# Optimization experiments

Measured on AMD Instinct MI355X. Metric: run time of the kernel, lower is better.

Reference implementation:

```python
import jax, jax.numpy as jnp
import numpy as np

B, T, D_IN, H1, H2, K = 16, 1024, 384, 1024, 1024, 9


def _l2normalize(w, axis):
    # matches F.normalize(w, dim=axis): w / max(||w||_2, 1e-12)
    n = jnp.sqrt(jnp.sum(w * w, axis=axis, keepdims=True))
    return w / jnp.maximum(n, 1e-12)


def _mish(x):
    return x * jnp.tanh(jax.nn.softplus(x))


def setup_inputs() -> dict:
    key = jax.random.key(0)
    ks = jax.random.split(key, 11)
    f32 = jnp.float32
    return {
        "input": jax.random.normal(ks[0], (B, T, D_IN), f32),
        "d_w": jax.random.normal(ks[1], (B, H1, 1, K), f32),
        "d_g": jax.random.normal(ks[2], (B, H1), f32),
        "d_b": jax.random.normal(ks[3], (B, H1), f32),
        "p_w": jax.random.normal(ks[4], (B, H1, H2, 1), f32),
        "p_g": jax.random.normal(ks[5], (B, H1), f32),
        "p_b": jax.random.normal(ks[6], (B, H2), f32),
        "w1_w": jax.random.normal(ks[7], (H1, D_IN), f32) * 0.05,
        "w1_b": jax.random.normal(ks[8], (H1,), f32) * 0.05,
        "w2_w": jax.random.normal(ks[9], (D_IN, H2), f32) * 0.05,
        "w2_b": jax.random.normal(ks[10], (D_IN,), f32) * 0.05,
    }


def reference(input, d_w, d_g, d_b, p_w, p_g, p_b, w1_w, w1_b, w2_w, w2_b):
    residual = input
    # w_1: 1x1 conv == per-position linear, then Mish (dropout = identity in eval)
    h = _mish(jnp.einsum('btc,hc->bth', input, w1_w) + w1_b)   # [B,T,H1]
    x = jnp.transpose(h, (0, 2, 1))                            # [B,H1,T]
    k = d_w.shape[-1]
    pad = (k - 1) // 2
    t = x.shape[-1]
    xp = jnp.pad(x, ((0, 0), (0, 0), (pad, pad)))              # [B,H1,T+2p]
    idx = jnp.arange(t)[:, None] + jnp.arange(k)[None, :]      # [T,K]
    xu = xp[:, :, idx]                                         # [B,H1,T,K] (unfold)
    # weight-normalized dynamic depthwise conv weights
    dwn = _l2normalize(d_w, axis=1) * d_g[:, :, None, None]    # [B,H1,1,K]
    # torch.einsum('bctk,bcwk->bct') with d_w expanded along w(=T): w is summed,
    # and every w-slice is identical, so the dot product picks up a factor of T.
    y = jnp.einsum('bctk,bck->bct', xu, dwn[:, :, 0, :]) * t   # [B,H1,T]
    y = y + d_b[:, :, None]
    # weight-normalized dynamic pointwise mix
    pwn = _l2normalize(p_w, axis=1) * p_g[:, :, None, None]    # [B,H1,H2,1]
    z = jnp.einsum('bct,bco->bot', y, pwn[..., 0])             # [B,H2,T]
    z = z + p_b[:, :, None]
    # w_2: 1x1 conv back to d_in, residual add
    out2 = jnp.einsum('bot,do->btd', z, w2_w) + w2_b           # [B,T,D_IN]
    return out2 + residual
```

## Files before the change

### kernel.cpp

```cpp
#include <hip/hip_runtime.h>

#define BCNT 16
#define TT 1024
#define DIN 384
#define H1 1024
#define H2 1024
#define KW 9

typedef __attribute__((ext_vector_type(8))) short bhalf8;
typedef __attribute__((ext_vector_type(4))) float f32x4;

typedef const __attribute__((address_space(1))) void* gas_ptr;
typedef __attribute__((address_space(3))) void* lds_ptr;

__device__ __forceinline__ float bf2f(unsigned short u) {
    return __uint_as_float(((unsigned int)u) << 16);
}
__device__ __forceinline__ unsigned short f2bf(float f) {
    unsigned int u = __float_as_uint(f);
    unsigned int r = (u + 0x7FFFu + ((u >> 16) & 1u)) >> 16;
    return (unsigned short)r;
}
__device__ __forceinline__ float mish_f(float x) {
    if (x > 20.f) return x;
    float u = __expf(x);
    float n = u * u + 2.f * u;
    return x * n / (n + 2.f);
}


__global__ __launch_bounds__(256) void k_cvt3z(
    const float* __restrict__ s0, unsigned short* __restrict__ d0, int n0,
    const float* __restrict__ s1, unsigned short* __restrict__ d1, int n1,
    const float* __restrict__ s2, unsigned short* __restrict__ d2, int n2,
    float* __restrict__ zb, int n3) {
    int i = blockIdx.x * 256 + threadIdx.x;
    const float* s; unsigned short* d; int j = i;
    if (i < n0) { s = s0; d = d0; }
    else if ((j = i - n0) < n1) { s = s1; d = d1; }
    else if ((j = i - n0 - n1) < n2) { s = s2; d = d2; }
    else if ((j = i - n0 - n1 - n2) < n3) {
        ((float4*)zb)[j] = make_float4(0.f, 0.f, 0.f, 0.f);
        return;
    } else return;
    float4 v = ((const float4*)s)[j];
    ushort4 o;
    o.x = f2bf(v.x); o.y = f2bf(v.y); o.z = f2bf(v.z); o.w = f2bf(v.w);
    ((ushort4*)d)[j] = o;
}

__global__ void k_norm_dwn(const float* __restrict__ d_w, const float* __restrict__ d_g,
                           float* __restrict__ dwn_s) {
    int idx = blockIdx.x;
    int b = idx / KW, k = idx % KW;
    float s = 0.f;
    for (int c = threadIdx.x; c < H1; c += 256) {
        float v = d_w[((size_t)b * H1 + c) * KW + k];
        s += v * v;
    }
    __shared__ float red[256];
    __shared__ float nsh;
    red[threadIdx.x] = s; __syncthreads();
    for (int st = 128; st > 0; st >>= 1) {
        if (threadIdx.x < st) red[threadIdx.x] += red[threadIdx.x + st];
        __syncthreads();
    }
    if (threadIdx.x == 0) nsh = fmaxf(sqrtf(red[0]), 1e-12f);
    __syncthreads();
    float n = nsh;
    for (int c = threadIdx.x; c < H1; c += 256) {
        size_t o = ((size_t)b * H1 + c) * KW + k;
        dwn_s[o] = d_w[o] / n * d_g[b * H1 + c] * (float)TT;
    }
}

__global__ __launch_bounds__(256) void k_tpw2(const float* __restrict__ p_w,
                                              const float* __restrict__ p_g,
                                              unsigned short* __restrict__ pwTu,
                                              float* __restrict__ sumsq) {
    __shared__ float tile[32][33];
    __shared__ float red[8][32];
    int tx = threadIdx.x & 31, ty = threadIdx.x >> 5;
    int c0 = blockIdx.x * 32, o0 = blockIdx.y * 32, b = blockIdx.z;
    float s = 0.f;
#pragma unroll
    for (int j = 0; j < 4; j++) {
        float v = p_w[((size_t)b * H1 + c0 + ty + j * 8) * H2 + o0 + tx];
        tile[ty + j * 8][tx] = v;
        s += v * v;
    }
    red[ty][tx] = s;
    __syncthreads();
    if (ty == 0) {
        float t = 0.f;
#pragma unroll
        for (int r = 0; r < 8; r++) t += red[r][tx];
        atomicAdd(&sumsq[(size_t)b * H2 + o0 + tx], t);
    }
#pragma unroll
    for (int j = 0; j < 4; j++) {
        int o = o0 + ty + j * 8, c = c0 + tx;
        float v = tile[tx][ty + j * 8] * p_g[(size_t)b * H1 + c];
        pwTu[((size_t)b * H2 + o) * H1 + c] = f2bf(v);
    }
}

__global__ __launch_bounds__(256) void k_conv(const unsigned short* __restrict__ h,
                                              const float* __restrict__ dwn_s,
                                              const float* __restrict__ d_b,
                                              unsigned short* __restrict__ y) {
    int tid = threadIdx.x;
    int c2 = blockIdx.y * 256 + tid;
    int c = c2 * 2;
    int t0 = blockIdx.x * 64;
    int b = blockIdx.z;
    const ushort2* hb = (const ushort2*)(h + (size_t)b * TT * H1);
    ushort2* yb = (ushort2*)(y + (size_t)b * TT * H1);
    float k0[KW], k1[KW];
#pragma unroll
    for (int i = 0; i < KW; i++) {
        k0[i] = dwn_s[((size_t)b * H1 + c) * KW + i];
        k1[i] = dwn_s[((size_t)b * H1 + c + 1) * KW + i];
    }
    float db0 = d_b[b * H1 + c], db1 = d_b[b * H1 + c + 1];
    float w0[KW], w1[KW];
#pragma unroll
    for (int i = 0; i < 8; i++) {
        int t = t0 - 4 + i;
        if (t >= 0 && t < TT) {
            ushort2 v = hb[(size_t)t * (H1 / 2) + c2];
            w0[i] = bf2f(v.x); w1[i] = bf2f(v.y);
        } else { w0[i] = 0.f; w1[i] = 0.f; }
    }
    for (int j = 0; j < 64; j++) {
        int t = t0 + j;
        int tl = t + 4;
        if (tl < TT) {
            ushort2 v = hb[(size_t)tl * (H1 / 2) + c2];
            w0[8] = bf2f(v.x); w1[8] = bf2f(v.y);
        } else { w0[8] = 0.f; w1[8] = 0.f; }
        float a0 = db0, a1 = db1;
#pragma unroll
        for (int i = 0; i < KW; i++) { a0 += k0[i] * w0[i]; a1 += k1[i] * w1[i]; }
        ushort2 o; o.x = f2bf(a0); o.y = f2bf(a1);
        yb[(size_t)t * (H1 / 2) + c2] = o;
#pragma unroll
        for (int i = 0; i < 8; i++) { w0[i] = w0[i + 1]; w1[i] = w1[i + 1]; }
    }
}

template <int MODE, int SWIZ, int TN>
__global__ __launch_bounds__(256, 4) void gemm_nt(
    const unsigned short* __restrict__ A, const unsigned short* __restrict__ Bm,
    void* __restrict__ Cp, int Kdim, int lda, int ldb, int ldc,
    long sA, long sB, long sC,
    const float* __restrict__ bias, int biasStride,
    const float* __restrict__ sumsq,
    const unsigned short* __restrict__ residbf) {
    constexpr int WN = TN / 32;
    __shared__ __attribute__((aligned(16))) unsigned short Al[128 * 64];
    __shared__ __attribute__((aligned(16))) unsigned short Bl[TN * 64];

    const int tid = threadIdx.x;
    const int lane = tid & 63, wv = tid >> 6;

    int bx, by, bz;
    if constexpr (SWIZ) {
        int l = blockIdx.x;
        int xcd = l & 7, s = l >> 3;
        bz = xcd * 2 + (s >> 6);
        int u = s & 63;
        bx = u & 7; by = u >> 3;
    } else {
        bx = blockIdx.x; by = blockIdx.y; bz = blockIdx.z;
    }
    const int bm = bx * 128, bn = by * TN;

    const unsigned short* Ab = A + (size_t)sA * bz;
    const unsigned short* Bb = Bm + (size_t)sB * bz;

    const int rS = lane >> 3;
    const int cS = ((lane & 7) ^ (rS & 7)) * 8;

    const int wm = (wv >> 1) * 64, wn = (wv & 1) * (TN / 2);
    const int l16 = lane & 15, quad = lane >> 4;
    const int fx = l16 & 7;

    f32x4 acc[4][WN];
#pragma unroll
    for (int i = 0; i < 4; i++)
#pragma unroll
        for (int j = 0; j < WN; j++)
#pragma unroll
            for (int r = 0; r < 4; r++) acc[i][j][r] = 0.f;

    const int ktiles = Kdim / 64;
    for (int kt = 0; kt < ktiles; ++kt) {
        const int kofs = kt * 64 + cS;
#pragma unroll
        for (int i = 0; i < 4; i++) {
            const int ch = i * 4 + wv;
            const unsigned short* ga = Ab + (size_t)(bm + ch * 8 + rS) * lda + kofs;
            __builtin_amdgcn_global_load_lds((gas_ptr)ga, (lds_ptr)&Al[ch * 512], 16, 0, 0);
        }
#pragma unroll
        for (int i = 0; i < TN / 32; i++) {
            const int ch = i * 4 + wv;
            const unsigned short* gb = Bb + (size_t)(bn + ch * 8 + rS) * ldb + kofs;
            __builtin_amdgcn_global_load_lds((gas_ptr)gb, (lds_ptr)&Bl[ch * 512], 16, 0, 0);
        }
        __syncthreads();

#pragma unroll
        for (int kk = 0; kk < 2; kk++) {
            const int cg = ((kk * 4 + quad) ^ fx) * 8;
            bhalf8 af[4], bf[WN];
#pragma unroll
            for (int mi = 0; mi < 4; mi++)
                af[mi] = *(const bhalf8*)&Al[(wm + mi * 16 + l16) * 64 + cg];
#pragma unroll
            for (int ni = 0; ni < WN; ni++)
                bf[ni] = *(const bhalf8*)&Bl[(wn + ni * 16 + l16) * 64 + cg];
#pragma unroll
            for (int mi = 0; mi < 4; mi++)
#pragma unroll
                for (int ni = 0; ni < WN; ni++)
                    acc[mi][ni] = __builtin_amdgcn_mfma_f32_16x16x32_bf16(af[mi], bf[ni],
                                                                         acc[mi][ni], 0, 0, 0);
        }
        __syncthreads();
    }

#pragma unroll
    for (int mi = 0; mi < 4; mi++)
#pragma unroll
        for (int ni = 0; ni < WN; ni++)
#pragma unroll
            for (int r = 0; r < 4; r++) {
                int gm = bm + wm + mi * 16 + quad * 4 + r;
                int gn = bn + wn + ni * 16 + l16;
                float v = acc[mi][ni][r];
                size_t cidx = (size_t)sC * bz + (size_t)gm * ldc + gn;
                if constexpr (MODE == 0) {
                    v = mish_f(v + bias[gn]);
                    ((unsigned short*)Cp)[cidx] = f2bf(v);
                } else if constexpr (MODE == 1) {
                    size_t si = (size_t)bz * biasStride + gn;
                    float rr = rsqrtf(fmaxf(sumsq[si], 1e-24f));
                    v = v * rr + bias[si];
                    ((unsigned short*)Cp)[cidx] = f2bf(v);
                } else {
                    v += bias[gn] + bf2f(residbf[cidx]);
                    ((float*)Cp)[cidx] = v;
                }
            }
}


extern "C" void kernel_launch(void* const* d_in, const int* in_sizes, int n_in,
                              void* d_out, int out_size, void* d_ws, size_t ws_size,
                              hipStream_t stream) {
    const float* input = (const float*)d_in[0];
    const float* d_w   = (const float*)d_in[1];
    const float* d_g   = (const float*)d_in[2];
    const float* d_b   = (const float*)d_in[3];
    const float* p_w   = (const float*)d_in[4];
    const float* p_g   = (const float*)d_in[5];
    const float* p_b   = (const float*)d_in[6];
    const float* w1_w  = (const float*)d_in[7];
    const float* w1_b  = (const float*)d_in[8];
    const float* w2_w  = (const float*)d_in[9];
    const float* w2_b  = (const float*)d_in[10];
    float* out = (float*)d_out;

    char* ws = (char*)d_ws;
    size_t off = 0;
    auto alloc = [&](size_t bytes) {
        char* p = ws + off;
        off += (bytes + 255) & ~(size_t)255;
        return p;
    };
    float* dwn_s         = (float*)alloc((size_t)BCNT * H1 * KW * 4);
    float* sumsq         = (float*)alloc((size_t)BCNT * H2 * 4);
    unsigned short* inbf = (unsigned short*)alloc((size_t)BCNT * TT * DIN * 2);
    unsigned short* w1bf = (unsigned short*)alloc((size_t)H1 * DIN * 2);
    unsigned short* w2bf = (unsigned short*)alloc((size_t)DIN * H2 * 2);
    unsigned short* h    = (unsigned short*)alloc((size_t)BCNT * TT * H1 * 2);
    unsigned short* y    = (unsigned short*)alloc((size_t)BCNT * TT * H1 * 2);
    unsigned short* pwTu = (unsigned short*)alloc((size_t)BCNT * H2 * H1 * 2);
    unsigned short* zt   = (unsigned short*)alloc((size_t)BCNT * TT * H2 * 2);

    const int n4_in = BCNT * TT * DIN / 4, n4_w1 = H1 * DIN / 4, n4_w2 = DIN * H2 / 4;
    const int n4_z = BCNT * H2 / 4;
    k_cvt3z<<<(n4_in + n4_w1 + n4_w2 + n4_z + 255) / 256, 256, 0, stream>>>(
        input, inbf, n4_in, w1_w, w1bf, n4_w1, w2_w, w2bf, n4_w2, sumsq, n4_z);

    k_norm_dwn<<<BCNT * KW, 256, 0, stream>>>(d_w, d_g, dwn_s);
    k_tpw2<<<dim3(H1 / 32, H2 / 32, BCNT), 256, 0, stream>>>(p_w, p_g, pwTu, sumsq);

    gemm_nt<0, 0, 128><<<dim3(BCNT * TT / 128, H1 / 128, 1), 256, 0, stream>>>(
        inbf, w1bf, h, DIN, DIN, DIN, H1, 0, 0, 0, w1_b, 0, nullptr, nullptr);

    k_conv<<<dim3(TT / 64, H1 / 512, BCNT), 256, 0, stream>>>(h, dwn_s, d_b, y);

    gemm_nt<1, 1, 128><<<dim3(1024, 1, 1), 256, 0, stream>>>(
        y, pwTu, zt, H1, H1, H1, H2, (long)TT * H1, (long)H2 * H1, (long)TT * H2,
        p_b, H2, sumsq, nullptr);

    gemm_nt<2, 0, 64><<<dim3(BCNT * TT / 128, DIN / 64, 1), 256, 0, stream>>>(
        zt, w2bf, out, H2, H2, H2, DIN, 0, 0, 0, w2_b, 0, nullptr, inbf);
}
```

Baseline: 276.4 us.

## Add dedicated first GEMM kernel with full-K B tile in LDS and direct A loads

Replaces the generic tiled GEMM for the input projection with a specialized kernel. Each block loads a 64-column slice of W1 covering the whole K=384 into swizzled LDS once, and each of its 8 waves computes a 64x64 tile, reading A fragments straight from global memory. An XCD-aware block mapping groups M-blocks for cache locality. This removes the per-K-step LDS staging and barriers for A, at the cost of uncoalesced-ish direct global A reads and higher register pressure from 16 accumulators.

```diff
diff --git a/kernel.cpp b/kernel.cpp
--- a/kernel.cpp
+++ b/kernel.cpp
@@ -149,6 +149,74 @@
     }
 }
 
+__global__ __launch_bounds__(512, 4) void gemm_g1(
+    const unsigned short* __restrict__ A, const unsigned short* __restrict__ Bm,
+    unsigned short* __restrict__ C, const float* __restrict__ bias) {
+    __shared__ __attribute__((aligned(16))) unsigned short Bl[64 * 384];
+
+    const int tid = threadIdx.x;
+    const int lane = tid & 63, wv = tid >> 6;
+
+    int l = blockIdx.x;
+    int xcd = l & 7, s = l >> 3;
+    int bx = xcd * 4 + (s & 3);
+    int by = s >> 2;
+    const int n0 = by * 64;
+
+    for (int i = tid; i < 64 * 48; i += 512) {
+        int n = i / 48, g = i % 48;
+        bhalf8 v = *(const bhalf8*)&Bm[(size_t)(n0 + n) * DIN + g * 8];
+        int p = (g & ~7) | ((g ^ n) & 7);
+        *(bhalf8*)&Bl[n * DIN + p * 8] = v;
+    }
+    __syncthreads();
+
+    const int l16 = lane & 15, quad = lane >> 4;
+    const int m0 = bx * 512 + wv * 64;
+
+    f32x4 acc[4][4];
+#pragma unroll
+    for (int i = 0; i < 4; i++)
+#pragma unroll
+        for (int j = 0; j < 4; j++)
+#pragma unroll
+            for (int r = 0; r < 4; r++) acc[i][j][r] = 0.f;
+
+    const unsigned short* Ab = A + (size_t)m0 * DIN + quad * 8;
+#pragma unroll
+    for (int kk = 0; kk < 12; kk++) {
+        bhalf8 af[4], bfr[4];
+#pragma unroll
+        for (int mi = 0; mi < 4; mi++)
+            af[mi] = *(const bhalf8*)&Ab[(size_t)(mi * 16 + l16) * DIN + kk * 32];
+#pragma unroll
+        for (int ni = 0; ni < 4; ni++) {
+            int n = ni * 16 + l16;
+            int g = kk * 4 + quad;
+            int p = (g & ~7) | ((g ^ n) & 7);
+            bfr[ni] = *(const bhalf8*)&Bl[n * DIN + p * 8];
+        }
+#pragma unroll
+        for (int mi = 0; mi < 4; mi++)
+#pragma unroll
+            for (int ni = 0; ni < 4; ni++)
+                acc[mi][ni] = __builtin_amdgcn_mfma_f32_16x16x32_bf16(af[mi], bfr[ni],
+                                                                     acc[mi][ni], 0, 0, 0);
+    }
+
+#pragma unroll
+    for (int mi = 0; mi < 4; mi++)
+#pragma unroll
+        for (int ni = 0; ni < 4; ni++)
+#pragma unroll
+            for (int r = 0; r < 4; r++) {
+                int gm = m0 + mi * 16 + quad * 4 + r;
+                int gn = n0 + ni * 16 + l16;
+                float v = mish_f(acc[mi][ni][r] + bias[gn]);
+                C[(size_t)gm * H1 + gn] = f2bf(v);
+            }
+}
+
 template <int MODE, int SWIZ, int TN>
 __global__ __launch_bounds__(256, 4) void gemm_nt(
     const unsigned short* __restrict__ A, const unsigned short* __restrict__ Bm,
@@ -298,8 +366,7 @@
     k_norm_dwn<<<BCNT * KW, 256, 0, stream>>>(d_w, d_g, dwn_s);
     k_tpw2<<<dim3(H1 / 32, H2 / 32, BCNT), 256, 0, stream>>>(p_w, p_g, pwTu, sumsq);
 
-    gemm_nt<0, 0, 128><<<dim3(BCNT * TT / 128, H1 / 128, 1), 256, 0, stream>>>(
-        inbf, w1bf, h, DIN, DIN, DIN, H1, 0, 0, 0, w1_b, 0, nullptr, nullptr);
+    gemm_g1<<<512, 512, 0, stream>>>(inbf, w1bf, h, w1_b);
 
     k_conv<<<dim3(TT / 64, H1 / 512, BCNT), 256, 0, stream>>>(h, dwn_s, d_b, y);
 
```

New measurement: 285.8 us. +3.4%, slower.

## Double-buffer LDS tiles in gemm_nt to overlap global loads with MFMA

Applied to the files above, without the earlier changes.

Splits the GEMM's A/B LDS tiles into two buffers and prefetches the next k-tile with global_load_lds while MFMAs run on the current one. Manual vmcnt waits and raw s_barrier replace __syncthreads, and s_setprio raises wave priority around the MFMA block. This targets exposed global-load latency in each k-iteration. LDS use doubles, so launch bounds drop to 2 or 3 blocks per CU, which lowers occupancy.

```diff
diff --git a/kernel.cpp b/kernel.cpp
--- a/kernel.cpp
+++ b/kernel.cpp
@@ -150,7 +150,7 @@
 }
 
 template <int MODE, int SWIZ, int TN>
-__global__ __launch_bounds__(256, 4) void gemm_nt(
+__global__ __launch_bounds__(256, TN == 128 ? 2 : 3) void gemm_nt(
     const unsigned short* __restrict__ A, const unsigned short* __restrict__ Bm,
     void* __restrict__ Cp, int Kdim, int lda, int ldb, int ldc,
     long sA, long sB, long sC,
@@ -158,8 +158,8 @@
     const float* __restrict__ sumsq,
     const unsigned short* __restrict__ residbf) {
     constexpr int WN = TN / 32;
-    __shared__ __attribute__((aligned(16))) unsigned short Al[128 * 64];
-    __shared__ __attribute__((aligned(16))) unsigned short Bl[TN * 64];
+    __shared__ __attribute__((aligned(16))) unsigned short Al[2][128 * 64];
+    __shared__ __attribute__((aligned(16))) unsigned short Bl[2][TN * 64];
 
     const int tid = threadIdx.x;
     const int lane = tid & 63, wv = tid >> 6;
@@ -194,22 +194,37 @@
 #pragma unroll
             for (int r = 0; r < 4; r++) acc[i][j][r] = 0.f;
 
-    const int ktiles = Kdim / 64;
-    for (int kt = 0; kt < ktiles; ++kt) {
+    auto STAGE = [&](int kt, int buf) {
         const int kofs = kt * 64 + cS;
 #pragma unroll
         for (int i = 0; i < 4; i++) {
             const int ch = i * 4 + wv;
             const unsigned short* ga = Ab + (size_t)(bm + ch * 8 + rS) * lda + kofs;
-            __builtin_amdgcn_global_load_lds((gas_ptr)ga, (lds_ptr)&Al[ch * 512], 16, 0, 0);
+            __builtin_amdgcn_global_load_lds((gas_ptr)ga, (lds_ptr)&Al[buf][ch * 512], 16, 0, 0);
         }
 #pragma unroll
         for (int i = 0; i < TN / 32; i++) {
             const int ch = i * 4 + wv;
             const unsigned short* gb = Bb + (size_t)(bn + ch * 8 + rS) * ldb + kofs;
-            __builtin_amdgcn_global_load_lds((gas_ptr)gb, (lds_ptr)&Bl[ch * 512], 16, 0, 0);
+            __builtin_amdgcn_global_load_lds((gas_ptr)gb, (lds_ptr)&Bl[buf][ch * 512], 16, 0, 0);
         }
-        __syncthreads();
+    };
+
+    const int ktiles = Kdim / 64;
+    int cur = 0;
+    STAGE(0, 0);
+
+    for (int kt = 0; kt < ktiles; ++kt) {
+        if (kt + 1 < ktiles) {
+            STAGE(kt + 1, cur ^ 1);
+            if constexpr (TN == 128)
+                asm volatile("s_waitcnt vmcnt(8)" ::: "memory");
+            else
+                asm volatile("s_waitcnt vmcnt(6)" ::: "memory");
+        } else {
+            asm volatile("s_waitcnt vmcnt(0)" ::: "memory");
+        }
+        __builtin_amdgcn_s_barrier();
 
 #pragma unroll
         for (int kk = 0; kk < 2; kk++) {
@@ -217,18 +232,23 @@
             bhalf8 af[4], bf[WN];
 #pragma unroll
             for (int mi = 0; mi < 4; mi++)
-                af[mi] = *(const bhalf8*)&Al[(wm + mi * 16 + l16) * 64 + cg];
+                af[mi] = *(const bhalf8*)&Al[cur][(wm + mi * 16 + l16) * 64 + cg];
 #pragma unroll
             for (int ni = 0; ni < WN; ni++)
-                bf[ni] = *(const bhalf8*)&Bl[(wn + ni * 16 + l16) * 64 + cg];
+                bf[ni] = *(const bhalf8*)&Bl[cur][(wn + ni * 16 + l16) * 64 + cg];
+            __builtin_amdgcn_s_setprio(1);
 #pragma unroll
             for (int mi = 0; mi < 4; mi++)
 #pragma unroll
                 for (int ni = 0; ni < WN; ni++)
                     acc[mi][ni] = __builtin_amdgcn_mfma_f32_16x16x32_bf16(af[mi], bf[ni],
                                                                          acc[mi][ni], 0, 0, 0);
+            __builtin_amdgcn_s_setprio(0);
         }
-        __syncthreads();
+        asm volatile("s_waitcnt lgkmcnt(0)" ::: "memory");
+        __builtin_amdgcn_sched_barrier(0);
+        __builtin_amdgcn_s_barrier();
+        cur ^= 1;
     }
 
 #pragma unroll
```

New measurement: 280.7 us. No clear change (+1.5%).

## Add 256x256-tile, 512-thread GEMM with 4-stage LDS pipeline for first two GEMMs

Applied to the files above, without the earlier changes.

Adds a new bf16 MFMA GEMM kernel that computes 256x256 output tiles with 8 waves, staging K-slices of 32 through a 4-slot LDS ring filled by direct global-to-LDS loads, with explicit vmcnt/lgkmcnt waits and scheduling barriers. It replaces the 128-tile GEMM for the input projection and for the batched pointwise-mix GEMM, using an XCD-aware block mapping. The aim is more operand reuse per LDS byte and better overlap of loads with MFMA work, at the cost of a larger register footprint, lower occupancy and only 256 blocks per launch.

```diff
diff --git a/kernel.cpp b/kernel.cpp
--- a/kernel.cpp
+++ b/kernel.cpp
@@ -149,6 +149,137 @@
     }
 }
 
+template <int MODE, int GS>
+__global__ __launch_bounds__(512, 2) void gemm256(
+    const unsigned short* __restrict__ A, const unsigned short* __restrict__ Bm,
+    unsigned short* __restrict__ Cp, int Kdim, int lda, int ldb, int ldc,
+    long sA, long sB, long sC,
+    const float* __restrict__ bias, int biasStride,
+    const float* __restrict__ sumsq) {
+    __shared__ __attribute__((aligned(16))) unsigned short Asl[4][256 * 32];
+    __shared__ __attribute__((aligned(16))) unsigned short Bsl[4][256 * 32];
+
+    const int tid = threadIdx.x;
+    const int lane = tid & 63, wv = tid >> 6;
+    const int wr = wv >> 2, wc = wv & 3;
+
+    int bx, by, bz;
+    {
+        int l = blockIdx.x;
+        int xcd = l & 7, s = l >> 3;
+        if constexpr (GS == 0) { bz = 0; bx = xcd * 8 + (s & 7); by = s >> 3; }
+        else { bz = xcd * 2 + (s >> 4); int u = s & 15; bx = u & 3; by = u >> 2; }
+    }
+    const int bm = bx * 256, bn = by * 256;
+    const unsigned short* Ab = A + (size_t)sA * bz;
+    const unsigned short* Bb = Bm + (size_t)sB * bz;
+
+    const int rS = lane >> 2;
+    const int gS = (lane & 3) ^ ((lane >> 3) & 3);
+
+    const int l16 = lane & 15, quad = lane >> 4;
+    const int sw = quad ^ ((l16 >> 1) & 3);
+    const int aoff = (wr * 128 + l16) * 32 + sw * 8;
+    const int boff = (wc * 64 + l16) * 32 + sw * 8;
+
+    f32x4 acc[8][4];
+#pragma unroll
+    for (int i = 0; i < 8; i++)
+#pragma unroll
+        for (int j = 0; j < 4; j++)
+#pragma unroll
+            for (int r = 0; r < 4; r++) acc[i][j][r] = 0.f;
+
+    auto STAGE = [&](int kt) {
+        const int slot = kt & 3;
+        const int kofs = kt * 32 + gS * 8;
+#pragma unroll
+        for (int i = 0; i < 2; i++) {
+            const int r0 = wv * 32 + i * 16;
+            const unsigned short* ga = Ab + (size_t)(bm + r0 + rS) * lda + kofs;
+            __builtin_amdgcn_global_load_lds((gas_ptr)ga, (lds_ptr)&Asl[slot][r0 * 32], 16, 0, 0);
+            const unsigned short* gb = Bb + (size_t)(bn + r0 + rS) * ldb + kofs;
+            __builtin_amdgcn_global_load_lds((gas_ptr)gb, (lds_ptr)&Bsl[slot][r0 * 32], 16, 0, 0);
+        }
+    };
+
+    const int nkt = Kdim / 32;
+    STAGE(0); STAGE(1); STAGE(2);
+
+    for (int kt = 0; kt < nkt; ++kt) {
+        if (kt + 3 < nkt) STAGE(kt + 3);
+        const int rem = nkt - 1 - kt;
+        if (rem >= 3)      asm volatile("s_waitcnt vmcnt(12)" ::: "memory");
+        else if (rem == 2) asm volatile("s_waitcnt vmcnt(8)" ::: "memory");
+        else if (rem == 1) asm volatile("s_waitcnt vmcnt(4)" ::: "memory");
+        else               asm volatile("s_waitcnt vmcnt(0)" ::: "memory");
+        __builtin_amdgcn_s_barrier();
+        asm volatile("" ::: "memory");
+
+        const unsigned short* As = Asl[kt & 3];
+        const unsigned short* Bs = Bsl[kt & 3];
+        bhalf8 af[8], bf[4];
+        bf[0] = *(const bhalf8*)&Bs[boff];
+        bf[1] = *(const bhalf8*)&Bs[boff + 512];
+        bf[2] = *(const bhalf8*)&Bs[boff + 1024];
+        bf[3] = *(const bhalf8*)&Bs[boff + 1536];
+        af[0] = *(const bhalf8*)&As[aoff];
+        af[1] = *(const bhalf8*)&As[aoff + 512];
+        __builtin_amdgcn_sched_barrier(0);
+        af[2] = *(const bhalf8*)&As[aoff + 2 * 512];
+        af[3] = *(const bhalf8*)&As[aoff + 3 * 512];
+        __builtin_amdgcn_sched_barrier(0);
+        af[4] = *(const bhalf8*)&As[aoff + 4 * 512];
+        af[5] = *(const bhalf8*)&As[aoff + 5 * 512];
+        __builtin_amdgcn_sched_barrier(0);
+        af[6] = *(const bhalf8*)&As[aoff + 6 * 512];
+        af[7] = *(const bhalf8*)&As[aoff + 7 * 512];
+        __builtin_amdgcn_sched_barrier(0);
+
+#pragma unroll
+        for (int q = 0; q < 4; q++) {
+            if (q == 0)      asm volatile("s_waitcnt lgkmcnt(6)" ::: "memory");
+            else if (q == 1) asm volatile("s_waitcnt lgkmcnt(4)" ::: "memory");
+            else if (q == 2) asm volatile("s_waitcnt lgkmcnt(2)" ::: "memory");
+            else             asm volatile("s_waitcnt lgkmcnt(0)" ::: "memory");
+            __builtin_amdgcn_sched_barrier(0);
+            __builtin_amdgcn_s_setprio(1);
+#pragma unroll
+            for (int ni = 0; ni < 4; ni++)
+                acc[2 * q][ni] = __builtin_amdgcn_mfma_f32_16x16x32_bf16(
+                    af[2 * q], bf[ni], acc[2 * q][ni], 0, 0, 0);
+#pragma unroll
+            for (int ni = 0; ni < 4; ni++)
+                acc[2 * q + 1][ni] = __builtin_amdgcn_mfma_f32_16x16x32_bf16(
+                    af[2 * q + 1], bf[ni], acc[2 * q + 1][ni], 0, 0, 0);
+            __builtin_amdgcn_s_setprio(0);
+        }
+        __builtin_amdgcn_s_barrier();
+        asm volatile("" ::: "memory");
+    }
+
+#pragma unroll
+    for (int mi = 0; mi < 8; mi++)
+#pragma unroll
+        for (int ni = 0; ni < 4; ni++)
+#pragma unroll
+            for (int r = 0; r < 4; r++) {
+                int gm = bm + wr * 128 + mi * 16 + quad * 4 + r;
+                int gn = bn + wc * 64 + ni * 16 + l16;
+                float v = acc[mi][ni][r];
+                size_t cidx = (size_t)sC * bz + (size_t)gm * ldc + gn;
+                if constexpr (MODE == 0) {
+                    v = mish_f(v + bias[gn]);
+                    Cp[cidx] = f2bf(v);
+                } else {
+                    size_t si = (size_t)bz * biasStride + gn;
+                    float rr = rsqrtf(fmaxf(sumsq[si], 1e-24f));
+                    v = v * rr + bias[si];
+                    Cp[cidx] = f2bf(v);
+                }
+            }
+}
+
 template <int MODE, int SWIZ, int TN>
 __global__ __launch_bounds__(256, 4) void gemm_nt(
     const unsigned short* __restrict__ A, const unsigned short* __restrict__ Bm,
@@ -298,14 +429,14 @@
     k_norm_dwn<<<BCNT * KW, 256, 0, stream>>>(d_w, d_g, dwn_s);
     k_tpw2<<<dim3(H1 / 32, H2 / 32, BCNT), 256, 0, stream>>>(p_w, p_g, pwTu, sumsq);
 
-    gemm_nt<0, 0, 128><<<dim3(BCNT * TT / 128, H1 / 128, 1), 256, 0, stream>>>(
-        inbf, w1bf, h, DIN, DIN, DIN, H1, 0, 0, 0, w1_b, 0, nullptr, nullptr);
+    gemm256<0, 0><<<256, 512, 0, stream>>>(
+        inbf, w1bf, h, DIN, DIN, DIN, H1, 0, 0, 0, w1_b, 0, nullptr);
 
     k_conv<<<dim3(TT / 64, H1 / 512, BCNT), 256, 0, stream>>>(h, dwn_s, d_b, y);
 
-    gemm_nt<1, 1, 128><<<dim3(1024, 1, 1), 256, 0, stream>>>(
+    gemm256<1, 1><<<256, 512, 0, stream>>>(
         y, pwTu, zt, H1, H1, H1, H2, (long)TT * H1, (long)H2 * H1, (long)TT * H2,
-        p_b, H2, sumsq, nullptr);
+        p_b, H2, sumsq);
 
     gemm_nt<2, 0, 64><<<dim3(BCNT * TT / 128, DIN / 64, 1), 256, 0, stream>>>(
         zt, w2bf, out, H2, H2, H2, DIN, 0, 0, 0, w2_b, 0, nullptr, inbf);
```

New measurement: 285.0 us. 1.03x slower.
